# Kernel optimization log

Hardware: AMD Instinct MI355X
Metric: run time of the kernel (lower is better)

Reference implementation:

```python
import jax, jax.numpy as jnp
import numpy as np

IN_FEATURES = 1024
OUT_FEATURES = 1024
GRID_SIZE = 5
SPLINE_ORDER = 3
GRID_RANGE = (-1.0, 1.0)


def make_grid():
    h = (GRID_RANGE[1] - GRID_RANGE[0]) / GRID_SIZE
    g = jnp.arange(-SPLINE_ORDER, GRID_SIZE + SPLINE_ORDER + 1, dtype=jnp.float32) * h + GRID_RANGE[0]
    return jnp.tile(g[None, :], (IN_FEATURES, 1))  # (in, G + 2k + 1)


def b_splines(x, grid):
    # x: (N, in), grid: (in, G+2k+1) -> bases: (N, in, G+k)
    xe = x[..., None]
    bases = ((xe >= grid[:, :-1]) & (xe < grid[:, 1:])).astype(x.dtype)
    for k in range(1, SPLINE_ORDER + 1):
        left = (xe - grid[:, :-(k + 1)]) / (grid[:, k:-1] - grid[:, :-(k + 1)])
        right = (grid[:, k + 1:] - xe) / (grid[:, k + 1:] - grid[:, 1:-k])
        bases = left * bases[:, :, :-1] + right * bases[:, :, 1:]
    return bases


def setup_inputs() -> dict:
    key = jax.random.key(0)
    k1, k2, k3 = jax.random.split(key, 3)
    x = jax.random.uniform(k1, (8192, IN_FEATURES), dtype=jnp.float32)
    # lecun_normal-style init: std = 1/sqrt(fan_in)
    base_weight = jax.random.normal(k2, (OUT_FEATURES, IN_FEATURES), dtype=jnp.float32) / np.sqrt(IN_FEATURES)
    coeff = GRID_SIZE + SPLINE_ORDER
    spline_weight = jax.random.normal(k3, (OUT_FEATURES, IN_FEATURES, coeff), dtype=jnp.float32) / np.sqrt(IN_FEATURES * coeff)
    spline_scaler = jnp.ones((OUT_FEATURES, IN_FEATURES), dtype=jnp.float32)
    grid = make_grid()
    return {"x": x, "grid": grid, "base_weight": base_weight,
            "spline_weight": spline_weight, "spline_scaler": spline_scaler}


def reference(x, grid, base_weight, spline_weight, spline_scaler):
    N = x.shape[0]
    base_out = jax.nn.silu(x) @ base_weight.T  # (N, out)
    bases = b_splines(x, grid)                 # (N, in, G+k)
    scaled_sw = spline_weight * spline_scaler[..., None]  # (out, in, G+k)
    spline_out = bases.reshape(N, -1) @ scaled_sw.reshape(OUT_FEATURES, -1).T  # (N, out)
    return base_out + spline_out
```

## Files before the change

### kernel.cpp

```cpp
#include <hip/hip_runtime.h>
#include <hip/hip_bf16.h>

#define IN_F 1024
#define OUT_F 1024
#define KTOT (IN_F * 9)
#define M_ROWS 8192

#define BK 64
#define NT (KTOT / BK)
#define NT_H (NT / 2)

#define A_TILE_E 16384
#define B_TILE_E 8192

typedef short bf16x8 __attribute__((ext_vector_type(8)));
typedef int   i32x4  __attribute__((ext_vector_type(4)));
typedef float f32x4  __attribute__((ext_vector_type(4)));

#define AS1 __attribute__((address_space(1)))
#define AS3 __attribute__((address_space(3)))

__device__ __forceinline__ void kan_basis_fast(
    float xv, const float* __restrict__ g,
    const float* __restrict__ inv1, const float* __restrict__ inv2,
    const float* __restrict__ inv3, float* __restrict__ out) {
  float b[11];
#pragma unroll
  for (int j = 0; j < 11; ++j)
    b[j] = (xv >= g[j] && xv < g[j + 1]) ? 1.0f : 0.0f;
#pragma unroll
  for (int j = 0; j < 10; ++j)
    b[j] = (xv - g[j]) * inv1[j] * b[j] + (g[j + 2] - xv) * inv1[j + 1] * b[j + 1];
#pragma unroll
  for (int j = 0; j < 9; ++j)
    b[j] = (xv - g[j]) * inv2[j] * b[j] + (g[j + 3] - xv) * inv2[j + 1] * b[j + 1];
#pragma unroll
  for (int j = 0; j < 8; ++j)
    b[j] = (xv - g[j]) * inv3[j] * b[j] + (g[j + 4] - xv) * inv3[j + 1] * b[j + 1];
#pragma unroll
  for (int j = 0; j < 8; ++j) out[j] = b[j];
}

__global__ __launch_bounds__(256) void expand_a(
    const float* __restrict__ x, const float* __restrict__ grid,
    __hip_bfloat16* __restrict__ A, int row0, int nrows) {
  const int tid = threadIdx.x;
  const int lane = tid & 63;
  const int wvx = tid >> 6;
  const int l15 = lane & 15;
  const int lhi = lane >> 4;

  const int nb = blockIdx.x >> 3;
  const int ib = blockIdx.x & 7;
  const int n_l = nb * 16 + l15;
  const int i0 = ib * 128 + wvx * 32 + lhi * 8;

  const int bm = n_l >> 8, wm = (n_l >> 6) & 3, m = (n_l >> 4) & 3;

  float g[12];
  const float* gp = grid + (size_t)i0 * 12;
#pragma unroll
  for (int j = 0; j < 12; ++j) g[j] = gp[j];
  float inv1[11], inv2[10], inv3[9];
#pragma unroll
  for (int j = 0; j < 11; ++j) inv1[j] = 1.0f / (g[j + 1] - g[j]);
#pragma unroll
  for (int j = 0; j < 10; ++j) inv2[j] = 1.0f / (g[j + 2] - g[j]);
#pragma unroll
  for (int j = 0; j < 9; ++j)  inv3[j] = 1.0f / (g[j + 3] - g[j]);

  const float* xp = x + (size_t)(row0 + n_l) * IN_F + i0;
  float xs[8];
  *(f32x4*)&xs[0] = *(const f32x4*)xp;
  *(f32x4*)&xs[4] = *(const f32x4*)(xp + 4);

  bf16x8 out[9];
#pragma unroll
  for (int j = 0; j < 8; ++j) {
    float xv = xs[j];
    float bas[8];
    kan_basis_fast(xv, g, inv1, inv2, inv3, bas);
    float s = xv / (1.0f + __expf(-xv));
    out[0][j] = (short)__bfloat16_as_ushort(__float2bfloat16(s));
#pragma unroll
    for (int c = 0; c < 8; ++c)
      out[c + 1][j] = (short)__bfloat16_as_ushort(__float2bfloat16(bas[c]));
  }

#pragma unroll
  for (int c = 0; c < 9; ++c) {
    int k0 = c * IN_F + i0;
    int kt = k0 >> 6;
    int kk = (k0 >> 5) & 1;
    size_t frag = ((((size_t)bm * NT + kt) * 4 + wm) * 4 + m) * 2 + kk;
    *(bf16x8*)(A + frag * 512 + lane * 8) = out[c];
  }
}

__global__ __launch_bounds__(256) void pack_b(
    const float* __restrict__ bw, const float* __restrict__ sw,
    const float* __restrict__ sc, __hip_bfloat16* __restrict__ B) {
  const int tid = threadIdx.x;
  const int lane = tid & 63;
  const int wid = blockIdx.x * 4 + (tid >> 6);
  const int og = wid >> 5;
  const int ib32 = wid & 31;
  const int obn = og >> 3, colg = og & 7;
  const int l15 = lane & 15, lhi = lane >> 4;
  const int o = og * 16 + l15;
  const int i0 = ib32 * 32 + lhi * 8;

  float bwv[8], scv[8];
  const float* bp = bw + (size_t)o * IN_F + i0;
  const float* sp = sc + (size_t)o * IN_F + i0;
  *(f32x4*)&bwv[0] = *(const f32x4*)bp;
  *(f32x4*)&bwv[4] = *(const f32x4*)(bp + 4);
  *(f32x4*)&scv[0] = *(const f32x4*)sp;
  *(f32x4*)&scv[4] = *(const f32x4*)(sp + 4);

  bf16x8 out[9];
#pragma unroll
  for (int j = 0; j < 8; ++j) {
    out[0][j] = (short)__bfloat16_as_ushort(__float2bfloat16(bwv[j]));
    const float* swp = sw + ((size_t)o * IN_F + i0 + j) * 8;
    float swv[8];
    *(f32x4*)&swv[0] = *(const f32x4*)swp;
    *(f32x4*)&swv[4] = *(const f32x4*)(swp + 4);
#pragma unroll
    for (int c = 0; c < 8; ++c)
      out[c + 1][j] = (short)__bfloat16_as_ushort(__float2bfloat16(swv[c] * scv[j]));
  }

#pragma unroll
  for (int c = 0; c < 9; ++c) {
    int kt = c * 16 + (ib32 >> 1);
    int kk = ib32 & 1;
    size_t frag = ((size_t)obn * NT + kt) * 16 + colg * 2 + kk;
    *(bf16x8*)(B + frag * 512 + lane * 8) = out[c];
  }
}


__device__ __forceinline__ void gld16(const __hip_bfloat16* g, __hip_bfloat16* l) {
  __builtin_amdgcn_global_load_lds((AS1 void*)g, (AS3 void*)l, 16, 0, 0);
}

#define DSRO(dst, addr, IMM)                                               \
  asm volatile("ds_read_b128 %0, %1 offset:" #IMM : "=v"(dst) : "v"(addr))

#define SB __builtin_amdgcn_sched_barrier(0)

#define READ_A8(d, aA) do {                                                \
    DSRO(d[0], aA, 0);     DSRO(d[1], aA, 1024);                           \
    DSRO(d[2], aA, 2048);  DSRO(d[3], aA, 3072);                           \
    DSRO(d[4], aA, 4096);  DSRO(d[5], aA, 5120);                           \
    DSRO(d[6], aA, 6144);  DSRO(d[7], aA, 7168);                           \
  } while (0)
#define READ_B4(d, bA) do {                                                \
    DSRO(d[0], bA, 0);     DSRO(d[1], bA, 1024);                           \
    DSRO(d[2], bA, 2048);  DSRO(d[3], bA, 3072);                           \
  } while (0)

#define MFMA32(sA, sB) do {                                                \
    __builtin_amdgcn_s_setprio(1);                                         \
    _Pragma("unroll")                                                      \
    for (int m_ = 0; m_ < 8; ++m_)                                         \
      _Pragma("unroll")                                                    \
      for (int n_ = 0; n_ < 4; ++n_)                                       \
        acc[m_][n_] = __builtin_amdgcn_mfma_f32_16x16x32_bf16(             \
            sA[m_], sB[n_], acc[m_][n_], 0, 0, 0);                         \
    __builtin_amdgcn_s_setprio(0);                                         \
  } while (0)

#define STAGE14(SLOT, GA_, GB_) do {                                       \
    __hip_bfloat16* d_ = ldsP + (SLOT) * 16384;                            \
    gld16(aPw + (GA_),         d_ + wv * 512);                             \
    gld16(aPw + (GA_) + 8192,  d_ + 4096 + wv * 512);                      \
    gld16(bP0w + (GB_),        d_ + 8192 + wv * 512);                      \
    gld16(bP1w + (GB_),        d_ + 12288 + wv * 512);                     \
  } while (0)

#define VM4 asm volatile("s_waitcnt vmcnt(4)" ::: "memory")
#define VM0 asm volatile("s_waitcnt vmcnt(0)" ::: "memory")
#define LGK0 asm volatile("s_waitcnt lgkmcnt(0)" ::: "memory")

#define BODY14(FA, FB, GA, GB, SN, STAGE_, VMW_) do {                      \
    STAGE_;                                                                \
    SB;                                                                    \
    VMW_;                                                                  \
    SB;                                                                    \
    LGK0;                                                                  \
    SB;                                                                    \
    __builtin_amdgcn_s_barrier();                                          \
    SB;                                                                    \
    READ_A8(GA, aRdB + (SN) * 32768u);                                     \
    READ_B4(GB, bRdB + (SN) * 32768u);                                     \
    SB;                                                                    \
    MFMA32(FA, FB);                                                        \
    SB;                                                                    \
  } while (0)

template <int ATOMIC>
__global__ __launch_bounds__(512, 2) void gemm_v14(
    const __hip_bfloat16* __restrict__ A, const __hip_bfloat16* __restrict__ B,
    float* __restrict__ C, float* __restrict__ P) {
  __shared__ __align__(16) __hip_bfloat16 S[4][16384];

  const int nwg = gridDim.x;
  const int q = nwg >> 3;
  const int L = (blockIdx.x & 7) * q + (blockIdx.x >> 3);
  const int bm = L >> 3;
  const int khalf = (L >> 2) & 1;
  const int bn2 = L & 3;

  const int tid = threadIdx.x;
  const int lane = tid & 63;
  const int wv = tid >> 6;
  const int wm = wv >> 2;
  const int wn = wv & 3;
  const int l15 = lane & 15, lhi = lane >> 4;

  const __hip_bfloat16* aPw =
      A + ((size_t)bm * NT + khalf * NT_H) * A_TILE_E + wv * 1024 + lane * 8;
  const __hip_bfloat16* bP0w =
      B + ((size_t)(2 * bn2) * NT + khalf * NT_H) * B_TILE_E + wv * 1024 + lane * 8;
  const __hip_bfloat16* bP1w =
      B + ((size_t)(2 * bn2 + 1) * NT + khalf * NT_H) * B_TILE_E + wv * 1024 + lane * 8;
  __hip_bfloat16* ldsP = &S[0][0];

  const uint32_t ldsB = (uint32_t)(uintptr_t)(AS3 const void*)&S[0][0];
  const uint32_t aRdB = ldsB + wm * 8192 + lane * 16;
  const uint32_t bRdB = ldsB + 16384 + wn * 4096 + lane * 16;

  f32x4 acc[8][4];
#pragma unroll
  for (int m = 0; m < 8; ++m)
#pragma unroll
    for (int n = 0; n < 4; ++n) acc[m][n] = f32x4{0.f, 0.f, 0.f, 0.f};

  bf16x8 fa[8], fb[4];
  bf16x8 ga[8], gb[4];

  STAGE14(0, 0, 0);
  STAGE14(1, 512, 512);
  VM4;
  SB;
  __builtin_amdgcn_s_barrier();
  SB;
  READ_A8(fa, aRdB);
  READ_B4(fb, bRdB);
  SB;
  aPw += 16384; bP0w += 8192; bP1w += 8192;

#pragma unroll 1
  for (int tt = 0; tt < 35; ++tt) {
    BODY14(fa, fb, ga, gb, 1, STAGE14(2, 0, 0), VM4);
    BODY14(ga, gb, fa, fb, 2, STAGE14(3, 512, 512), VM4);
    BODY14(fa, fb, ga, gb, 3, STAGE14(0, 16384, 8192), VM4);
    BODY14(ga, gb, fa, fb, 0, STAGE14(1, 16896, 8704), VM4);
    aPw += 32768; bP0w += 16384; bP1w += 16384;
  }
  BODY14(fa, fb, ga, gb, 1, STAGE14(2, 0, 0), VM4);
  BODY14(ga, gb, fa, fb, 2, STAGE14(3, 512, 512), VM4);
  BODY14(fa, fb, ga, gb, 3, ;, VM0);
  LGK0;
  SB;
  MFMA32(ga, gb);

  if (ATOMIC) {
#pragma unroll
    for (int m = 0; m < 8; ++m)
#pragma unroll
      for (int n = 0; n < 4; ++n) {
        int col = bn2 * 256 + wn * 64 + n * 16 + l15;
        int row0 = bm * 256 + wm * 128 + m * 16 + lhi * 4;
#pragma unroll
        for (int j = 0; j < 4; ++j)
          atomicAdd(&C[(size_t)(row0 + j) * OUT_F + col], acc[m][n][j]);
      }
  } else if (khalf == 1) {
#pragma unroll
    for (int m = 0; m < 8; ++m)
#pragma unroll
      for (int n = 0; n < 4; ++n) {
        int col = bn2 * 256 + wn * 64 + n * 16 + l15;
        int row0 = bm * 256 + wm * 128 + m * 16 + lhi * 4;
#pragma unroll
        for (int j = 0; j < 4; ++j)
          C[(size_t)(row0 + j) * OUT_F + col] = acc[m][n][j];
      }
  } else {
    float* Pt = P + (size_t)(bm * 4 + bn2) * 65536;
    int cl = wn * 64 + l15;
    int rl = wm * 128 + lhi * 4;
#pragma unroll
    for (int m = 0; m < 8; ++m)
#pragma unroll
      for (int n = 0; n < 4; ++n)
#pragma unroll
        for (int j = 0; j < 4; ++j)
          Pt[(size_t)(rl + m * 16 + j) * 256 + cl + n * 16] = acc[m][n][j];
  }
}

__global__ __launch_bounds__(256) void reduce2(
    const float* __restrict__ P, float* __restrict__ C) {
  const int NG = M_ROWS * OUT_F / 4;
  for (int g = blockIdx.x * 256 + threadIdx.x; g < NG; g += gridDim.x * 256) {
    int row = g >> 8;
    int c4 = g & 255;
    int bm = row >> 8, bn2 = c4 >> 6;
    int r = row & 255, cl = (c4 & 63) * 4;
    f32x4 p = *(const f32x4*)(P + (size_t)(bm * 4 + bn2) * 65536 + r * 256 + cl);
    f32x4* o = (f32x4*)(C + (size_t)row * OUT_F + c4 * 4);
    *o += p;
  }
}

__global__ __launch_bounds__(256) void kan_naive(
    const float* __restrict__ x, const float* __restrict__ grid,
    const float* __restrict__ bw, const float* __restrict__ sw,
    const float* __restrict__ sc, float* __restrict__ out) {
  __shared__ float s_act[IN_F];
  __shared__ float s_bas[IN_F * 8];
  int n = blockIdx.x;
  for (int i = threadIdx.x; i < IN_F; i += 256) {
    float xv = x[(size_t)n * IN_F + i];
    float g[12];
    const float* gp = grid + i * 12;
#pragma unroll
    for (int t = 0; t < 12; ++t) g[t] = gp[t];
    float b[11];
#pragma unroll
    for (int j = 0; j < 11; ++j)
      b[j] = (xv >= g[j] && xv < g[j + 1]) ? 1.0f : 0.0f;
#pragma unroll
    for (int k = 1; k <= 3; ++k)
#pragma unroll
      for (int j = 0; j < 11 - k; ++j) {
        float left = (xv - g[j]) / (g[j + k] - g[j]);
        float right = (g[j + k + 1] - xv) / (g[j + k + 1] - g[j + 1]);
        b[j] = left * b[j] + right * b[j + 1];
      }
    s_act[i] = xv / (1.0f + __expf(-xv));
#pragma unroll
    for (int c = 0; c < 8; ++c) s_bas[i * 8 + c] = b[c];
  }
  __syncthreads();
  for (int o = threadIdx.x; o < OUT_F; o += 256) {
    float acc = 0.f;
    const float* bwo = bw + (size_t)o * IN_F;
    const float* swo = sw + (size_t)o * IN_F * 8;
    const float* sco = sc + (size_t)o * IN_F;
    for (int i = 0; i < IN_F; ++i) {
      acc += s_act[i] * bwo[i];
      float p = 0.f;
#pragma unroll
      for (int c = 0; c < 8; ++c) p += s_bas[i * 8 + c] * swo[i * 8 + c];
      acc += p * sco[i];
    }
    out[(size_t)n * OUT_F + o] = acc;
  }
}

extern "C" void kernel_launch(void* const* d_in, const int* in_sizes, int n_in,
                              void* d_out, int out_size, void* d_ws, size_t ws_size,
                              hipStream_t stream) {
  const float* x  = (const float*)d_in[0];
  const float* grid = (const float*)d_in[1];
  const float* bw = (const float*)d_in[2];
  const float* sw = (const float*)d_in[3];
  const float* sc = (const float*)d_in[4];
  float* out = (float*)d_out;

  const size_t Bbytes = (size_t)OUT_F * KTOT * 2;
  const size_t Abytes = (size_t)M_ROWS * KTOT * 2;
  const size_t Pbytes = (size_t)32 * 4 * 65536 * 4;
  const size_t rowBytes = (size_t)KTOT * 2;

  if (ws_size >= Bbytes + Abytes + Pbytes) {
    __hip_bfloat16* Bp = (__hip_bfloat16*)d_ws;
    __hip_bfloat16* Ap = (__hip_bfloat16*)((char*)d_ws + Bbytes);
    float* Pp = (float*)((char*)d_ws + Bbytes + Abytes);

    pack_b<<<OUT_F * 128 / 256, 256, 0, stream>>>(bw, sw, sc, Bp);
    expand_a<<<(M_ROWS / 16) * 8, 256, 0, stream>>>(x, grid, Ap, 0, M_ROWS);
    gemm_v14<0><<<(M_ROWS / 256) * 8, 512, 0, stream>>>(Ap, Bp, out, Pp);
    reduce2<<<2048, 256, 0, stream>>>(Pp, out);
  } else if (ws_size >= Bbytes + 256 * rowBytes) {
    __hip_bfloat16* Bp = (__hip_bfloat16*)d_ws;
    __hip_bfloat16* Ap = (__hip_bfloat16*)((char*)d_ws + Bbytes);
    size_t arows = (ws_size - Bbytes) / rowBytes;
    int chunk = (int)((arows / 256) * 256);
    if (chunk > M_ROWS) chunk = M_ROWS;

    hipMemsetAsync(d_out, 0, (size_t)out_size * sizeof(float), stream);
    pack_b<<<OUT_F * 128 / 256, 256, 0, stream>>>(bw, sw, sc, Bp);
    for (int r0 = 0; r0 < M_ROWS; r0 += chunk) {
      int rows = M_ROWS - r0 < chunk ? M_ROWS - r0 : chunk;
      expand_a<<<(rows / 16) * 8, 256, 0, stream>>>(x, grid, Ap, r0, rows);
      gemm_v14<1><<<(rows / 256) * 8, 512, 0, stream>>>(Ap, Bp,
                                                        out + (size_t)r0 * OUT_F,
                                                        (float*)Ap );
    }
  } else {
    kan_naive<<<M_ROWS, 256, 0, stream>>>(x, grid, bw, sw, sc, out);
  }
}
```

Measured before the change: 192.4 us.

## Restructure GEMM main loop into double-step with one barrier per two K-tiles

The main loop now processes two K-tiles per step. It issues two global-to-LDS stages up front, reads the next LDS fragments while running MFMAs on the current ones (using a partial lgkmcnt wait), and waits for all outstanding loads with vmcnt(0) before a single barrier per pair of tiles. This halves the barrier count and overlaps LDS reads with MFMA issue. In exchange, the wait for global loads is now fully blocking (vmcnt 0 instead of 4), which shortens the prefetch distance and may expose memory latency.

```diff
diff --git a/kernel.cpp b/kernel.cpp
--- a/kernel.cpp
+++ b/kernel.cpp
@@ -172,7 +172,7 @@
     __builtin_amdgcn_s_setprio(0);                                         \
   } while (0)
 
-#define STAGE14(SLOT, GA_, GB_) do {                                       \
+#define STAGE15(SLOT, GA_, GB_) do {                                       \
     __hip_bfloat16* d_ = ldsP + (SLOT) * 16384;                            \
     gld16(aPw + (GA_),         d_ + wv * 512);                             \
     gld16(aPw + (GA_) + 8192,  d_ + 4096 + wv * 512);                      \
@@ -180,28 +180,31 @@
     gld16(bP1w + (GB_),        d_ + 12288 + wv * 512);                     \
   } while (0)
 
-#define VM4 asm volatile("s_waitcnt vmcnt(4)" ::: "memory")
 #define VM0 asm volatile("s_waitcnt vmcnt(0)" ::: "memory")
 #define LGK0 asm volatile("s_waitcnt lgkmcnt(0)" ::: "memory")
-
-#define BODY14(FA, FB, GA, GB, SN, STAGE_, VMW_) do {                      \
-    STAGE_;                                                                \
+#define LGK12 asm volatile("s_waitcnt lgkmcnt(12)" ::: "memory")
+
+#define DSTEP(S1_, S2_, S3_, GA_, GB_) do {                                \
+    STAGE15(S2_, (GA_), (GB_));                                            \
+    STAGE15(S3_, (GA_) + 512, (GB_) + 512);                                \
+    READ_A8(ga, aRdB + (S1_) * 32768u);                                    \
+    READ_B4(gb, bRdB + (S1_) * 32768u);                                    \
     SB;                                                                    \
-    VMW_;                                                                  \
+    LGK12; SB;                                                             \
+    MFMA32(fa, fb);                                                        \
     SB;                                                                    \
-    LGK0;                                                                  \
+    LGK0; SB;                                                              \
+    MFMA32(ga, gb);                                                        \
     SB;                                                                    \
-    __builtin_amdgcn_s_barrier();                                          \
-    SB;                                                                    \
-    READ_A8(GA, aRdB + (SN) * 32768u);                                     \
-    READ_B4(GB, bRdB + (SN) * 32768u);                                     \
-    SB;                                                                    \
-    MFMA32(FA, FB);                                                        \
+    VM0; SB;                                                               \
+    __builtin_amdgcn_s_barrier(); SB;                                      \
+    READ_A8(fa, aRdB + (S2_) * 32768u);                                    \
+    READ_B4(fb, bRdB + (S2_) * 32768u);                                    \
     SB;                                                                    \
   } while (0)
 
 template <int ATOMIC>
-__global__ __launch_bounds__(512, 2) void gemm_v14(
+__global__ __launch_bounds__(512, 2) void gemm_v15(
     const __hip_bfloat16* __restrict__ A, const __hip_bfloat16* __restrict__ B,
     float* __restrict__ C, float* __restrict__ P) {
   __shared__ __align__(16) __hip_bfloat16 S[4][16384];
@@ -241,12 +244,10 @@
   bf16x8 fa[8], fb[4];
   bf16x8 ga[8], gb[4];
 
-  STAGE14(0, 0, 0);
-  STAGE14(1, 512, 512);
-  VM4;
-  SB;
-  __builtin_amdgcn_s_barrier();
-  SB;
+  STAGE15(0, 0, 0);
+  STAGE15(1, 512, 512);
+  VM0; SB;
+  __builtin_amdgcn_s_barrier(); SB;
   READ_A8(fa, aRdB);
   READ_B4(fb, bRdB);
   SB;
@@ -254,18 +255,20 @@
 
 #pragma unroll 1
   for (int tt = 0; tt < 35; ++tt) {
-    BODY14(fa, fb, ga, gb, 1, STAGE14(2, 0, 0), VM4);
-    BODY14(ga, gb, fa, fb, 2, STAGE14(3, 512, 512), VM4);
-    BODY14(fa, fb, ga, gb, 3, STAGE14(0, 16384, 8192), VM4);
-    BODY14(ga, gb, fa, fb, 0, STAGE14(1, 16896, 8704), VM4);
+    DSTEP(1, 2, 3, 0, 0);
+    DSTEP(3, 0, 1, 16384, 8192);
     aPw += 32768; bP0w += 16384; bP1w += 16384;
   }
-  BODY14(fa, fb, ga, gb, 1, STAGE14(2, 0, 0), VM4);
-  BODY14(ga, gb, fa, fb, 2, STAGE14(3, 512, 512), VM4);
-  BODY14(fa, fb, ga, gb, 3, ;, VM0);
-  LGK0;
+  DSTEP(1, 2, 3, 0, 0);
+  READ_A8(ga, aRdB + 3 * 32768u);
+  READ_B4(gb, bRdB + 3 * 32768u);
   SB;
+  LGK12; SB;
+  MFMA32(fa, fb);
+  SB;
+  LGK0; SB;
   MFMA32(ga, gb);
+  SB;
 
   if (ATOMIC) {
 #pragma unroll
@@ -385,7 +388,7 @@
 
     pack_b<<<OUT_F * 128 / 256, 256, 0, stream>>>(bw, sw, sc, Bp);
     expand_a<<<(M_ROWS / 16) * 8, 256, 0, stream>>>(x, grid, Ap, 0, M_ROWS);
-    gemm_v14<0><<<(M_ROWS / 256) * 8, 512, 0, stream>>>(Ap, Bp, out, Pp);
+    gemm_v15<0><<<(M_ROWS / 256) * 8, 512, 0, stream>>>(Ap, Bp, out, Pp);
     reduce2<<<2048, 256, 0, stream>>>(Pp, out);
   } else if (ws_size >= Bbytes + 256 * rowBytes) {
     __hip_bfloat16* Bp = (__hip_bfloat16*)d_ws;
@@ -399,7 +402,7 @@
     for (int r0 = 0; r0 < M_ROWS; r0 += chunk) {
       int rows = M_ROWS - r0 < chunk ? M_ROWS - r0 : chunk;
       expand_a<<<(rows / 16) * 8, 256, 0, stream>>>(x, grid, Ap, r0, rows);
-      gemm_v14<1><<<(rows / 256) * 8, 512, 0, stream>>>(Ap, Bp,
+      gemm_v15<1><<<(rows / 256) * 8, 512, 0, stream>>>(Ap, Bp,
                                                         out + (size_t)r0 * OUT_F,
                                                         (float*)Ap );
     }
```

Result: no change. 192.3 us (-0.1%).
